# Kernel optimization log

Hardware: AMD Instinct MI355X
Metric: run time of the kernel (lower is better)

## Reference

```python
import jax, jax.numpy as jnp
import numpy as np

B, H, W, C, FD, HID = 64, 128, 128, 10, 32, 64
OFFSETS = [(-1,-1),(-1,0),(-1,1),(0,-1),(0,1),(1,-1),(1,0),(1,1)]

def setup_inputs() -> dict:
    key = jax.random.key(0)
    ks = jax.random.split(key, 13)
    s = lambda n: 1.0 / np.sqrt(n)
    return {
        "beliefs": jax.random.normal(ks[0], (B, H, W, C), jnp.float32),
        "constraints": jax.random.uniform(ks[1], (B, H, W, 8, 3), jnp.float32),
        "filename_embed": jax.random.normal(ks[2], (B, FD), jnp.float32),
        # message_net: Linear(2C+3+FD -> HID), ReLU, Linear(HID -> C)
        "mw1": jax.random.uniform(ks[3], (2*C+3+FD, HID), jnp.float32, -s(2*C+3+FD), s(2*C+3+FD)),
        "mb1": jax.random.uniform(ks[4], (HID,), jnp.float32, -s(2*C+3+FD), s(2*C+3+FD)),
        "mw2": jax.random.uniform(ks[5], (HID, C), jnp.float32, -s(HID), s(HID)),
        "mb2": jax.random.uniform(ks[6], (C,), jnp.float32, -s(HID), s(HID)),
        # update_net: Linear(2C -> HID), ReLU, Linear(HID -> C)
        "uw1": jax.random.uniform(ks[7], (2*C, HID), jnp.float32, -s(2*C), s(2*C)),
        "ub1": jax.random.uniform(ks[8], (HID,), jnp.float32, -s(2*C), s(2*C)),
        "uw2": jax.random.uniform(ks[9], (HID, C), jnp.float32, -s(HID), s(HID)),
        "ub2": jax.random.uniform(ks[10], (C,), jnp.float32, -s(HID), s(HID)),
        "gamma": jnp.ones((C,), jnp.float32),
        "beta": jnp.zeros((C,), jnp.float32),
    }

def reference(beliefs, constraints, filename_embed, mw1, mb1, mw2, mb2, uw1, ub1, uw2, ub2, gamma, beta):
    b, h, w, c = beliefs.shape
    # replicate-pad spatial dims (matches F.pad mode='replicate')
    bp = jnp.pad(beliefs, ((0,0),(1,1),(1,1),(0,0)), mode='edge')
    # gather 8 neighbors -> [B,H,W,8,C]
    neigh = jnp.stack([bp[:, 1+dy:1+dy+h, 1+dx:1+dx+w, :] for dy, dx in OFFSETS], axis=3)
    self_b = jnp.broadcast_to(beliefs[:, :, :, None, :], (b, h, w, 8, c))
    fn = jnp.broadcast_to(filename_embed[:, None, None, None, :], (b, h, w, 8, filename_embed.shape[-1]))
    msg_in = jnp.concatenate([self_b, neigh, constraints, fn], axis=-1)  # [B,H,W,8,2C+3+FD]
    msgs = jax.nn.relu(msg_in @ mw1 + mb1) @ mw2 + mb2                   # [B,H,W,8,C]
    agg = msgs.mean(axis=3)                                              # [B,H,W,C]
    upd_in = jnp.concatenate([beliefs, agg], axis=-1)
    upd = jax.nn.relu(upd_in @ uw1 + ub1) @ uw2 + ub2
    x = beliefs + 0.5 * upd
    mu = x.mean(-1, keepdims=True)
    var = ((x - mu) ** 2).mean(-1, keepdims=True)
    return (x - mu) * jax.lax.rsqrt(var + 1e-5) * gamma + beta
```

## Files before the change

### kernel.cpp

```cpp
#include <hip/hip_runtime.h>
#include <hip/hip_bf16.h>

typedef unsigned int u32;
typedef _Float16 h2 __attribute__((ext_vector_type(2)));

#define TILE 16
#define HALO 18
#define NPIX (HALO*HALO)
#define NBSTRIDE 36

#define W_SELF   0
#define W_NBW    320
#define W_WC     640
#define W_MW2    736
#define W_UB1    1056
#define W_UW1    1088
#define W_UW2    1728
#define WS_W     2048
#define WS_SCAL  4096
#define WS_DWORDS 4136

__device__ __forceinline__ h2 pkrtz(float a, float b) {
    return __builtin_bit_cast(h2, __builtin_amdgcn_cvt_pkrtz(a, b));
}
#if __has_builtin(__builtin_elementwise_fma)
__device__ __forceinline__ h2 pkfma(h2 a, h2 b, h2 c) { return __builtin_elementwise_fma(a, b, c); }
#else
extern "C" __device__ h2 __ocml_fma_2f16(h2, h2, h2);
__device__ __forceinline__ h2 pkfma(h2 a, h2 b, h2 c) { return __ocml_fma_2f16(a, b, c); }
#endif
__device__ __forceinline__ float dot2f(h2 a, h2 b, float c) {
#if __has_builtin(__builtin_amdgcn_fdot2)
    return __builtin_amdgcn_fdot2(__builtin_bit_cast(__attribute__((ext_vector_type(2))) __fp16, a),
                                  __builtin_bit_cast(__attribute__((ext_vector_type(2))) __fp16, b),
                                  c, false);
#else
    return fmaf((float)a.x, (float)b.x, fmaf((float)a.y, (float)b.y, c));
#endif
}
__device__ __forceinline__ h2 relu2(h2 v) {
    h2 z = (h2)(_Float16)0;
#if __has_builtin(__builtin_elementwise_max)
    return __builtin_elementwise_max(v, z);
#else
    h2 r;
    r.x = v.x > (_Float16)0 ? v.x : (_Float16)0;
    r.y = v.y > (_Float16)0 ? v.y : (_Float16)0;
    return r;
#endif
}
__device__ __forceinline__ h2 h2cast(u32 v) { return __builtin_bit_cast(h2, v); }

__global__ __launch_bounds__(64) void prep_kernel(
    const float* __restrict__ fn,  const float* __restrict__ mw1, const float* __restrict__ mb1,
    const float* __restrict__ mw2, const float* __restrict__ mb2, const float* __restrict__ uw1,
    const float* __restrict__ ub1, const float* __restrict__ uw2, const float* __restrict__ ub2,
    const float* __restrict__ gam, const float* __restrict__ bet, u32* __restrict__ ws)
{
    const int b = blockIdx.x, t = threadIdx.x;
    h2* wh = (h2*)ws;
    if (t < 32) {
        float a0 = mb1[2*t], a1 = mb1[2*t+1];
        for (int f = 0; f < 32; f++) {
            float fv = fn[b*32 + f];
            a0 += fv * mw1[(23+f)*64 + 2*t];
            a1 += fv * mw1[(23+f)*64 + 2*t+1];
        }
        wh[b*32 + t] = pkrtz(a0, a1);
    }
    if (b == 0) {
        for (int i = t; i < 2048; i += 64) {
            float a, c; int j;
            if      (i < 320)  { int cc = i>>5,  hp = i&31;  a = mw1[cc*64 + 2*hp];       c = mw1[cc*64 + 2*hp+1]; }
            else if (i < 640)  { j = i-320;  int q = j>>6, hh = j&63; a = mw1[(10+2*q)*64 + hh]; c = mw1[(11+2*q)*64 + hh]; }
            else if (i < 736)  { j = i-640;  int r = j>>5, hp = j&31; a = mw1[(20+r)*64 + 2*hp]; c = mw1[(20+r)*64 + 2*hp+1]; }
            else if (i < 1056) { j = i-736;  int cc = j>>5, hp = j&31; a = mw2[(2*hp)*10 + cc];  c = mw2[(2*hp+1)*10 + cc]; }
            else if (i < 1088) { j = i-1056; a = ub1[2*j]; c = ub1[2*j+1]; }
            else if (i < 1728) { j = i-1088; int cc = j>>5, hp = j&31; a = uw1[cc*64 + 2*hp];    c = uw1[cc*64 + 2*hp+1]; }
            else               { j = i-1728; int cc = j>>5, hp = j&31; a = uw2[(2*hp)*10 + cc];  c = uw2[(2*hp+1)*10 + cc]; }
            wh[WS_W + i] = pkrtz(a, c);
        }
        if (t < 40) {
            float v;
            if      (t < 10) v = mb2[t];
            else if (t < 20) v = ub2[t-10];
            else if (t < 30) v = gam[t-20];
            else             v = bet[t-30];
            ((float*)ws)[WS_SCAL + t] = v;
        }
    }
}

__global__ __launch_bounds__(256, 3) void mp_kernel(
    const float* __restrict__ beliefs, const float* __restrict__ cons,
    const u32* __restrict__ ws, float* __restrict__ out)
{
    __shared__ h2 bel_s[NPIX*5];
    __shared__ __align__(16) u32 nbp_u[NPIX*NBSTRIDE];

    const int tid = threadIdx.x;
    const int b = blockIdx.z, y0 = blockIdx.y*TILE, x0 = blockIdx.x*TILE;

    const h2* Wfnb = (const h2*)ws;
    const h2* W    = ((const h2*)ws) + WS_W;
    const float* SC = ((const float*)ws) + WS_SCAL;

    for (int i = tid; i < NPIX*5; i += 256) {
        int p = i/5, q = i - p*5;
        int py = p/HALO, px = p - py*HALO;
        int gy = y0-1+py; gy = gy<0?0:(gy>127?127:gy);
        int gx = x0-1+px; gx = gx<0?0:(gx>127?127:gx);
        const float2 v = *(const float2*)(beliefs + (size_t)((b*128+gy)*128+gx)*10 + 2*q);
        bel_s[i] = pkrtz(v.x, v.y);
    }
    __syncthreads();

    for (int p = tid; p < NPIX; p += 256) {
        h2 bc[5];
        #pragma unroll
        for (int q = 0; q < 5; q++) bc[q] = bel_s[p*5 + q];
        #pragma unroll 4
        for (int hp = 0; hp < 32; hp++) {
            float a0 = 0.f, a1 = 0.f;
            #pragma unroll
            for (int q = 0; q < 5; q++) {
                a0 = dot2f(bc[q], W[W_NBW + q*64 + 2*hp],     a0);
                a1 = dot2f(bc[q], W[W_NBW + q*64 + 2*hp + 1], a1);
            }
            nbp_u[p*NBSTRIDE + hp] = __builtin_bit_cast(u32, pkrtz(a0, a1));
        }
    }
    __syncthreads();

    const int tx = tid & 15, ty = tid >> 4;
    const int pc = (ty+1)*HALO + (tx+1);
    const size_t gpix = (size_t)((b*128 + (y0+ty))*128 + (x0+tx));

    int p36[8];
    {
        const int doff[8] = {-19,-18,-17,-1,1,17,18,19};
        #pragma unroll
        for (int k = 0; k < 8; k++) p36[k] = (pc + doff[k]) * NBSTRIDE;
    }

    float bel[10]; h2 beld[10];
    {
        const float2* bp = (const float2*)(beliefs + gpix*10);
        #pragma unroll
        for (int q = 0; q < 5; q++) {
            float2 v = bp[q];
            bel[2*q] = v.x; bel[2*q+1] = v.y;
            beld[2*q]   = pkrtz(v.x, v.x);
            beld[2*q+1] = pkrtz(v.y, v.y);
        }
    }
    h2 cond[24];
    {
        const float4* cp = (const float4*)(cons + gpix*24);
        #pragma unroll
        for (int r = 0; r < 6; r++) {
            float4 v = cp[r];
            cond[4*r+0] = pkrtz(v.x, v.x);
            cond[4*r+1] = pkrtz(v.y, v.y);
            cond[4*r+2] = pkrtz(v.z, v.z);
            cond[4*r+3] = pkrtz(v.w, v.w);
        }
    }

    float acc2[10];
    #pragma unroll
    for (int c = 0; c < 10; c++) acc2[c] = 0.f;

    #pragma unroll 2
    for (int ch = 0; ch < 8; ch++) {
        const int hb = 4*ch;
        h2 t01[4], s01[4];
        #pragma unroll
        for (int j = 0; j < 4; j++) { t01[j] = Wfnb[b*32 + hb + j]; s01[j] = (h2)(_Float16)0; }
        #pragma unroll
        for (int c = 0; c < 10; c++) {
            #pragma unroll
            for (int j = 0; j < 4; j++)
                t01[j] = pkfma(beld[c], W[W_SELF + c*32 + hb + j], t01[j]);
        }
        h2 wc0[4], wc1[4], wc2[4];
        #pragma unroll
        for (int j = 0; j < 4; j++) {
            wc0[j] = W[W_WC      + hb + j];
            wc1[j] = W[W_WC + 32 + hb + j];
            wc2[j] = W[W_WC + 64 + hb + j];
        }
        #pragma unroll
        for (int k = 0; k < 8; k++) {
            const uint4 nv = *(const uint4*)(nbp_u + p36[k] + hb);
            const h2 nb[4] = { h2cast(nv.x), h2cast(nv.y), h2cast(nv.z), h2cast(nv.w) };
            const h2 c0 = cond[k*3+0], c1 = cond[k*3+1], c2 = cond[k*3+2];
            #pragma unroll
            for (int j = 0; j < 4; j++) {
                h2 v = t01[j] + nb[j];
                v = pkfma(c0, wc0[j], v);
                v = pkfma(c1, wc1[j], v);
                v = pkfma(c2, wc2[j], v);
                s01[j] += relu2(v);
            }
        }
        #pragma unroll
        for (int c = 0; c < 10; c++) {
            #pragma unroll
            for (int j = 0; j < 4; j++)
                acc2[c] = dot2f(s01[j], W[W_MW2 + c*32 + hb + j], acc2[c]);
        }
    }

    h2 aggd[10];
    #pragma unroll
    for (int c = 0; c < 10; c++) {
        float a = acc2[c]*0.125f + SC[c];
        aggd[c] = pkrtz(a, a);
    }

    float od[10];
    #pragma unroll
    for (int c = 0; c < 10; c++) od[c] = 0.f;

    #pragma unroll 4
    for (int hp = 0; hp < 32; hp++) {
        h2 u01 = W[W_UB1 + hp];
        #pragma unroll
        for (int c = 0; c < 10; c++) u01 = pkfma(beld[c], W[W_UW1 + c*32 + hp], u01);
        #pragma unroll
        for (int c = 0; c < 10; c++) u01 = pkfma(aggd[c], W[W_UW1 + (10+c)*32 + hp], u01);
        u01 = relu2(u01);
        #pragma unroll
        for (int c = 0; c < 10; c++) od[c] = dot2f(u01, W[W_UW2 + c*32 + hp], od[c]);
    }

    float x[10], mu = 0.f;
    #pragma unroll
    for (int c = 0; c < 10; c++) { x[c] = bel[c] + 0.5f*(od[c] + SC[10+c]); mu += x[c]; }
    mu *= 0.1f;
    float var = 0.f;
    #pragma unroll
    for (int c = 0; c < 10; c++) { float d = x[c] - mu; var += d*d; }
    var *= 0.1f;
    const float rs = rsqrtf(var + 1e-5f);

    float2* op = (float2*)(out + gpix*10);
    #pragma unroll
    for (int q = 0; q < 5; q++) {
        float2 r;
        r.x = (x[2*q]   - mu)*rs*SC[20+2*q]   + SC[30+2*q];
        r.y = (x[2*q+1] - mu)*rs*SC[20+2*q+1] + SC[30+2*q+1];
        op[q] = r;
    }
}

__device__ __forceinline__ float bf_lo(u32 v) { return __uint_as_float(v << 16); }
__device__ __forceinline__ float bf_hi(u32 v) { return __uint_as_float(v & 0xffff0000u); }
__device__ __forceinline__ u32 f2bf(float f) {
    u32 u = __float_as_uint(f);
    return (u + 0x7fffu + ((u >> 16) & 1u)) >> 16;
}
__device__ __forceinline__ u32 pack2(float a, float b) { return f2bf(a) | (f2bf(b) << 16); }
__device__ __forceinline__ u32 fpair(const float* a, int pi) { return pack2(a[2*pi], a[2*pi+1]); }

#define FW_MW2 736
#define FW_MB2 1056
#define FW_UW1 1061
#define FW_UB1 1701
#define FW_UW2 1733
#define FW_UB2 2053
#define FW_GAM 2058
#define FW_BET 2063
#define FW_TOT 2068

__global__ __launch_bounds__(256) void fallback_kernel(
    const float* __restrict__ beliefs, const float* __restrict__ cons, const float* __restrict__ fn,
    const float* __restrict__ mw1, const float* __restrict__ mb1, const float* __restrict__ mw2,
    const float* __restrict__ mb2, const float* __restrict__ uw1, const float* __restrict__ ub1,
    const float* __restrict__ uw2, const float* __restrict__ ub2, const float* __restrict__ gam,
    const float* __restrict__ bet, float* __restrict__ out)
{
    __shared__ float bel_s[NPIX*10];
    __shared__ u32   nbp_s[32*NPIX];
    __shared__ u32   w_s[FW_TOT];
    __shared__ float fnb_s[64];

    const int tid = threadIdx.x;
    const int b  = blockIdx.z;
    const int y0 = blockIdx.y * TILE;
    const int x0 = blockIdx.x * TILE;

    for (int i = tid; i < FW_TOT; i += 256) {
        u32 v;
        if      (i < 736)  v = fpair(mw1, i);
        else if (i < 1056) v = fpair(mw2, i - 736);
        else if (i < 1061) v = fpair(mb2, i - 1056);
        else if (i < 1701) v = fpair(uw1, i - 1061);
        else if (i < 1733) v = fpair(ub1, i - 1701);
        else if (i < 2053) v = fpair(uw2, i - 1733);
        else if (i < 2058) v = fpair(ub2, i - 2053);
        else if (i < 2063) v = fpair(gam, i - 2058);
        else               v = fpair(bet, i - 2063);
        w_s[i] = v;
    }
    if (tid < 64) {
        float acc = mb1[tid];
        #pragma unroll 8
        for (int f = 0; f < 32; f++)
            acc += fn[b*32 + f] * mw1[(23 + f)*64 + tid];
        fnb_s[tid] = acc;
    }
    for (int idx = tid; idx < NPIX*10; idx += 256) {
        int p = idx/10, c = idx - p*10;
        int py = p/HALO, px = p - py*HALO;
        int gy = y0-1+py; gy = gy<0?0:(gy>127?127:gy);
        int gx = x0-1+px; gx = gx<0?0:(gx>127?127:gx);
        bel_s[idx] = beliefs[((size_t)(b*128+gy)*128+gx)*10 + c];
    }
    __syncthreads();

    for (int p = tid; p < NPIX; p += 256) {
        float bl[10];
        #pragma unroll
        for (int c = 0; c < 10; c++) bl[c] = bel_s[p*10 + c];
        #pragma unroll 4
        for (int hp = 0; hp < 32; hp++) {
            float t0 = 0.f, t1 = 0.f;
            #pragma unroll
            for (int c = 0; c < 10; c++) {
                u32 wv = w_s[(10 + c)*32 + hp];
                t0 += bl[c] * bf_lo(wv);
                t1 += bl[c] * bf_hi(wv);
            }
            nbp_s[hp*NPIX + p] = pack2(t0, t1);
        }
    }
    __syncthreads();

    const int tx = tid & 15, ty = tid >> 4;
    const int pc = (ty + 1)*HALO + (tx + 1);
    float bel[10];
    #pragma unroll
    for (int c = 0; c < 10; c++) bel[c] = bel_s[pc*10 + c];
    const size_t gpix = (size_t)(b*128 + (y0 + ty))*128 + (x0 + tx);
    float con[24];
    #pragma unroll
    for (int j = 0; j < 24; j++) con[j] = cons[gpix*24 + j];

    float acc2[10];
    #pragma unroll
    for (int c = 0; c < 10; c++) acc2[c] = 0.f;

    #pragma unroll 2
    for (int hp = 0; hp < 32; hp++) {
        const int h0 = 2*hp, h1 = h0 + 1;
        float t0 = fnb_s[h0], t1 = fnb_s[h1];
        #pragma unroll
        for (int c = 0; c < 10; c++) {
            u32 wv = w_s[c*32 + hp];
            t0 += bel[c] * bf_lo(wv);
            t1 += bel[c] * bf_hi(wv);
        }
        const u32 wc0 = w_s[20*32 + hp], wc1 = w_s[21*32 + hp], wc2 = w_s[22*32 + hp];
        const u32* nbb = nbp_s + hp*NPIX + pc - 19;
        float s0 = 0.f, s1 = 0.f;
        #pragma unroll
        for (int k = 0; k < 8; k++) {
            const int doff[8] = { 0, 1, 2, 18, 20, 36, 37, 38 };
            u32 nv = nbb[doff[k]];
            float c0 = con[k*3], c1 = con[k*3+1], c2 = con[k*3+2];
            float v0 = t0 + bf_lo(nv) + c0*bf_lo(wc0) + c1*bf_lo(wc1) + c2*bf_lo(wc2);
            float v1 = t1 + bf_hi(nv) + c0*bf_hi(wc0) + c1*bf_hi(wc1) + c2*bf_hi(wc2);
            s0 += fmaxf(v0, 0.f);
            s1 += fmaxf(v1, 0.f);
        }
        #pragma unroll
        for (int cq = 0; cq < 5; cq++) {
            u32 a0 = w_s[FW_MW2 + h0*5 + cq];
            u32 a1 = w_s[FW_MW2 + h1*5 + cq];
            acc2[2*cq]   += s0*bf_lo(a0) + s1*bf_lo(a1);
            acc2[2*cq+1] += s0*bf_hi(a0) + s1*bf_hi(a1);
        }
    }

    float agg[10];
    #pragma unroll
    for (int cq = 0; cq < 5; cq++) {
        u32 bp = w_s[FW_MB2 + cq];
        agg[2*cq]   = acc2[2*cq]  *0.125f + bf_lo(bp);
        agg[2*cq+1] = acc2[2*cq+1]*0.125f + bf_hi(bp);
    }

    float od[10];
    #pragma unroll
    for (int c = 0; c < 10; c++) od[c] = 0.f;
    #pragma unroll 2
    for (int hp = 0; hp < 32; hp++) {
        u32 ubp = w_s[FW_UB1 + hp];
        float u0 = bf_lo(ubp), u1 = bf_hi(ubp);
        #pragma unroll
        for (int c = 0; c < 10; c++) {
            u32 wv = w_s[FW_UW1 + c*32 + hp];
            u0 += bel[c] * bf_lo(wv);
            u1 += bel[c] * bf_hi(wv);
        }
        #pragma unroll
        for (int c = 0; c < 10; c++) {
            u32 wv = w_s[FW_UW1 + (10 + c)*32 + hp];
            u0 += agg[c] * bf_lo(wv);
            u1 += agg[c] * bf_hi(wv);
        }
        u0 = fmaxf(u0, 0.f); u1 = fmaxf(u1, 0.f);
        const int h0 = 2*hp, h1 = h0 + 1;
        #pragma unroll
        for (int cq = 0; cq < 5; cq++) {
            u32 a0 = w_s[FW_UW2 + h0*5 + cq];
            u32 a1 = w_s[FW_UW2 + h1*5 + cq];
            od[2*cq]   += u0*bf_lo(a0) + u1*bf_lo(a1);
            od[2*cq+1] += u0*bf_hi(a0) + u1*bf_hi(a1);
        }
    }

    float x[10], mu = 0.f;
    #pragma unroll
    for (int cq = 0; cq < 5; cq++) {
        u32 bp = w_s[FW_UB2 + cq];
        x[2*cq]   = bel[2*cq]   + 0.5f*(od[2*cq]   + bf_lo(bp));
        x[2*cq+1] = bel[2*cq+1] + 0.5f*(od[2*cq+1] + bf_hi(bp));
        mu += x[2*cq] + x[2*cq+1];
    }
    mu *= 0.1f;
    float var = 0.f;
    #pragma unroll
    for (int c = 0; c < 10; c++) { float d = x[c] - mu; var += d*d; }
    var *= 0.1f;
    const float rs = rsqrtf(var + 1e-5f);

    float2* op = reinterpret_cast<float2*>(out + gpix*10);
    #pragma unroll
    for (int q = 0; q < 5; q++) {
        u32 gp = w_s[FW_GAM + q], bq = w_s[FW_BET + q];
        float2 r;
        r.x = (x[2*q]   - mu)*rs*bf_lo(gp) + bf_lo(bq);
        r.y = (x[2*q+1] - mu)*rs*bf_hi(gp) + bf_hi(bq);
        op[q] = r;
    }
}

extern "C" void kernel_launch(void* const* d_in, const int* in_sizes, int n_in,
                              void* d_out, int out_size, void* d_ws, size_t ws_size,
                              hipStream_t stream) {
    (void)in_sizes; (void)n_in; (void)out_size;
    const float* beliefs = (const float*)d_in[0];
    const float* cons    = (const float*)d_in[1];
    const float* fn      = (const float*)d_in[2];
    const float* mw1     = (const float*)d_in[3];
    const float* mb1     = (const float*)d_in[4];
    const float* mw2     = (const float*)d_in[5];
    const float* mb2     = (const float*)d_in[6];
    const float* uw1     = (const float*)d_in[7];
    const float* ub1     = (const float*)d_in[8];
    const float* uw2     = (const float*)d_in[9];
    const float* ub2     = (const float*)d_in[10];
    const float* gam     = (const float*)d_in[11];
    const float* bet     = (const float*)d_in[12];
    float* outp = (float*)d_out;

    if (ws_size >= (size_t)WS_DWORDS*4) {
        prep_kernel<<<dim3(64), dim3(64), 0, stream>>>(
            fn, mw1, mb1, mw2, mb2, uw1, ub1, uw2, ub2, gam, bet, (u32*)d_ws);
        mp_kernel<<<dim3(8, 8, 64), dim3(256), 0, stream>>>(
            beliefs, cons, (const u32*)d_ws, outp);
    } else {
        fallback_kernel<<<dim3(8, 8, 64), dim3(256), 0, stream>>>(
            beliefs, cons, fn, mw1, mb1, mw2, mb2, uw1, ub1, uw2, ub2, gam, bet, outp);
    }
}
```

Baseline: 321.1 us.

## Split neighbor projection into two hidden halves to cut LDS and raise occupancy

The shared neighbor-projection buffer is restructured into a chunk-major layout holding only half of the hidden units at a time. It is computed and consumed in two passes with a barrier between them, and the bel_s staging buffer is dropped by reading halo beliefs straight from global memory. The smaller LDS footprint lets launch bounds target 6 blocks per CU instead of 3. The prep kernel also spreads weight packing across all blocks instead of block 0. The cost is halo beliefs being loaded twice, extra barriers, and more register pressure under the tighter occupancy bound.

```diff
diff --git a/kernel.cpp b/kernel.cpp
--- a/kernel.cpp
+++ b/kernel.cpp
@@ -7,7 +7,6 @@
 #define TILE 16
 #define HALO 18
 #define NPIX (HALO*HALO)
-#define NBSTRIDE 36
 
 #define W_SELF   0
 #define W_NBW    320
@@ -61,42 +60,40 @@
     h2* wh = (h2*)ws;
     if (t < 32) {
         float a0 = mb1[2*t], a1 = mb1[2*t+1];
+        #pragma unroll 8
         for (int f = 0; f < 32; f++) {
             float fv = fn[b*32 + f];
             a0 += fv * mw1[(23+f)*64 + 2*t];
             a1 += fv * mw1[(23+f)*64 + 2*t+1];
         }
         wh[b*32 + t] = pkrtz(a0, a1);
-    }
-    if (b == 0) {
-        for (int i = t; i < 2048; i += 64) {
-            float a, c; int j;
-            if      (i < 320)  { int cc = i>>5,  hp = i&31;  a = mw1[cc*64 + 2*hp];       c = mw1[cc*64 + 2*hp+1]; }
-            else if (i < 640)  { j = i-320;  int q = j>>6, hh = j&63; a = mw1[(10+2*q)*64 + hh]; c = mw1[(11+2*q)*64 + hh]; }
-            else if (i < 736)  { j = i-640;  int r = j>>5, hp = j&31; a = mw1[(20+r)*64 + 2*hp]; c = mw1[(20+r)*64 + 2*hp+1]; }
-            else if (i < 1056) { j = i-736;  int cc = j>>5, hp = j&31; a = mw2[(2*hp)*10 + cc];  c = mw2[(2*hp+1)*10 + cc]; }
-            else if (i < 1088) { j = i-1056; a = ub1[2*j]; c = ub1[2*j+1]; }
-            else if (i < 1728) { j = i-1088; int cc = j>>5, hp = j&31; a = uw1[cc*64 + 2*hp];    c = uw1[cc*64 + 2*hp+1]; }
-            else               { j = i-1728; int cc = j>>5, hp = j&31; a = uw2[(2*hp)*10 + cc];  c = uw2[(2*hp+1)*10 + cc]; }
-            wh[WS_W + i] = pkrtz(a, c);
-        }
-        if (t < 40) {
-            float v;
-            if      (t < 10) v = mb2[t];
-            else if (t < 20) v = ub2[t-10];
-            else if (t < 30) v = gam[t-20];
-            else             v = bet[t-30];
-            ((float*)ws)[WS_SCAL + t] = v;
-        }
-    }
-}
-
-__global__ __launch_bounds__(256, 3) void mp_kernel(
+    } else {
+        const int i = b*32 + (t - 32);
+        float a, c; int j;
+        if      (i < 320)  { int cc = i>>5,  hp = i&31;  a = mw1[cc*64 + 2*hp];       c = mw1[cc*64 + 2*hp+1]; }
+        else if (i < 640)  { j = i-320;  int q = j>>6, hh = j&63; a = mw1[(10+2*q)*64 + hh]; c = mw1[(11+2*q)*64 + hh]; }
+        else if (i < 736)  { j = i-640;  int r = j>>5, hp = j&31; a = mw1[(20+r)*64 + 2*hp]; c = mw1[(20+r)*64 + 2*hp+1]; }
+        else if (i < 1056) { j = i-736;  int cc = j>>5, hp = j&31; a = mw2[(2*hp)*10 + cc];  c = mw2[(2*hp+1)*10 + cc]; }
+        else if (i < 1088) { j = i-1056; a = ub1[2*j]; c = ub1[2*j+1]; }
+        else if (i < 1728) { j = i-1088; int cc = j>>5, hp = j&31; a = uw1[cc*64 + 2*hp];    c = uw1[cc*64 + 2*hp+1]; }
+        else               { j = i-1728; int cc = j>>5, hp = j&31; a = uw2[(2*hp)*10 + cc];  c = uw2[(2*hp+1)*10 + cc]; }
+        wh[WS_W + i] = pkrtz(a, c);
+    }
+    if (b == 0 && t < 40) {
+        float v;
+        if      (t < 10) v = mb2[t];
+        else if (t < 20) v = ub2[t-10];
+        else if (t < 30) v = gam[t-20];
+        else             v = bet[t-30];
+        ((float*)ws)[WS_SCAL + t] = v;
+    }
+}
+
+__global__ __launch_bounds__(256, 6) void mp_kernel(
     const float* __restrict__ beliefs, const float* __restrict__ cons,
     const u32* __restrict__ ws, float* __restrict__ out)
 {
-    __shared__ h2 bel_s[NPIX*5];
-    __shared__ __align__(16) u32 nbp_u[NPIX*NBSTRIDE];
+    __shared__ __align__(16) u32 nbp_u[4*NPIX*4];
 
     const int tid = threadIdx.x;
     const int b = blockIdx.z, y0 = blockIdx.y*TILE, x0 = blockIdx.x*TILE;
@@ -105,42 +102,15 @@
     const h2* W    = ((const h2*)ws) + WS_W;
     const float* SC = ((const float*)ws) + WS_SCAL;
 
-    for (int i = tid; i < NPIX*5; i += 256) {
-        int p = i/5, q = i - p*5;
-        int py = p/HALO, px = p - py*HALO;
-        int gy = y0-1+py; gy = gy<0?0:(gy>127?127:gy);
-        int gx = x0-1+px; gx = gx<0?0:(gx>127?127:gx);
-        const float2 v = *(const float2*)(beliefs + (size_t)((b*128+gy)*128+gx)*10 + 2*q);
-        bel_s[i] = pkrtz(v.x, v.y);
-    }
-    __syncthreads();
-
-    for (int p = tid; p < NPIX; p += 256) {
-        h2 bc[5];
-        #pragma unroll
-        for (int q = 0; q < 5; q++) bc[q] = bel_s[p*5 + q];
-        #pragma unroll 4
-        for (int hp = 0; hp < 32; hp++) {
-            float a0 = 0.f, a1 = 0.f;
-            #pragma unroll
-            for (int q = 0; q < 5; q++) {
-                a0 = dot2f(bc[q], W[W_NBW + q*64 + 2*hp],     a0);
-                a1 = dot2f(bc[q], W[W_NBW + q*64 + 2*hp + 1], a1);
-            }
-            nbp_u[p*NBSTRIDE + hp] = __builtin_bit_cast(u32, pkrtz(a0, a1));
-        }
-    }
-    __syncthreads();
-
     const int tx = tid & 15, ty = tid >> 4;
     const int pc = (ty+1)*HALO + (tx+1);
     const size_t gpix = (size_t)((b*128 + (y0+ty))*128 + (x0+tx));
 
-    int p36[8];
+    int pnb[8];
     {
         const int doff[8] = {-19,-18,-17,-1,1,17,18,19};
         #pragma unroll
-        for (int k = 0; k < 8; k++) p36[k] = (pc + doff[k]) * NBSTRIDE;
+        for (int k = 0; k < 8; k++) pnb[k] = pc + doff[k];
     }
 
     float bel[10]; h2 beld[10];
@@ -171,44 +141,75 @@
     #pragma unroll
     for (int c = 0; c < 10; c++) acc2[c] = 0.f;
 
-    #pragma unroll 2
-    for (int ch = 0; ch < 8; ch++) {
-        const int hb = 4*ch;
-        h2 t01[4], s01[4];
-        #pragma unroll
-        for (int j = 0; j < 4; j++) { t01[j] = Wfnb[b*32 + hb + j]; s01[j] = (h2)(_Float16)0; }
-        #pragma unroll
-        for (int c = 0; c < 10; c++) {
-            #pragma unroll
-            for (int j = 0; j < 4; j++)
-                t01[j] = pkfma(beld[c], W[W_SELF + c*32 + hb + j], t01[j]);
-        }
-        h2 wc0[4], wc1[4], wc2[4];
-        #pragma unroll
-        for (int j = 0; j < 4; j++) {
-            wc0[j] = W[W_WC      + hb + j];
-            wc1[j] = W[W_WC + 32 + hb + j];
-            wc2[j] = W[W_WC + 64 + hb + j];
-        }
-        #pragma unroll
-        for (int k = 0; k < 8; k++) {
-            const uint4 nv = *(const uint4*)(nbp_u + p36[k] + hb);
-            const h2 nb[4] = { h2cast(nv.x), h2cast(nv.y), h2cast(nv.z), h2cast(nv.w) };
-            const h2 c0 = cond[k*3+0], c1 = cond[k*3+1], c2 = cond[k*3+2];
+    for (int half = 0; half < 2; half++) {
+        if (half) __syncthreads();
+
+        for (int p = tid; p < NPIX; p += 256) {
+            int py = p/HALO, px = p - py*HALO;
+            int gy = y0-1+py; gy = gy<0?0:(gy>127?127:gy);
+            int gx = x0-1+px; gx = gx<0?0:(gx>127?127:gx);
+            const float2* bp = (const float2*)(beliefs + (size_t)((b*128+gy)*128+gx)*10);
+            h2 bc[5];
+            #pragma unroll
+            for (int q = 0; q < 5; q++) { float2 v = bp[q]; bc[q] = pkrtz(v.x, v.y); }
+            #pragma unroll
+            for (int cl = 0; cl < 4; cl++) {
+                u32 ov[4];
+                #pragma unroll
+                for (int j = 0; j < 4; j++) {
+                    const int hp = half*16 + cl*4 + j;
+                    float a0 = 0.f, a1 = 0.f;
+                    #pragma unroll
+                    for (int q = 0; q < 5; q++) {
+                        a0 = dot2f(bc[q], W[W_NBW + q*64 + 2*hp],     a0);
+                        a1 = dot2f(bc[q], W[W_NBW + q*64 + 2*hp + 1], a1);
+                    }
+                    ov[j] = __builtin_bit_cast(u32, pkrtz(a0, a1));
+                }
+                *(uint4*)(nbp_u + ((cl*NPIX + p) << 2)) = make_uint4(ov[0], ov[1], ov[2], ov[3]);
+            }
+        }
+        __syncthreads();
+
+        #pragma unroll 2
+        for (int cl = 0; cl < 4; cl++) {
+            const int hb = half*16 + cl*4;
+            h2 t01[4], s01[4];
+            #pragma unroll
+            for (int j = 0; j < 4; j++) { t01[j] = Wfnb[b*32 + hb + j]; s01[j] = (h2)(_Float16)0; }
+            #pragma unroll
+            for (int c = 0; c < 10; c++) {
+                #pragma unroll
+                for (int j = 0; j < 4; j++)
+                    t01[j] = pkfma(beld[c], W[W_SELF + c*32 + hb + j], t01[j]);
+            }
+            h2 wc0[4], wc1[4], wc2[4];
             #pragma unroll
             for (int j = 0; j < 4; j++) {
-                h2 v = t01[j] + nb[j];
-                v = pkfma(c0, wc0[j], v);
-                v = pkfma(c1, wc1[j], v);
-                v = pkfma(c2, wc2[j], v);
-                s01[j] += relu2(v);
-            }
-        }
-        #pragma unroll
-        for (int c = 0; c < 10; c++) {
-            #pragma unroll
-            for (int j = 0; j < 4; j++)
-                acc2[c] = dot2f(s01[j], W[W_MW2 + c*32 + hb + j], acc2[c]);
+                wc0[j] = W[W_WC      + hb + j];
+                wc1[j] = W[W_WC + 32 + hb + j];
+                wc2[j] = W[W_WC + 64 + hb + j];
+            }
+            #pragma unroll
+            for (int k = 0; k < 8; k++) {
+                const uint4 nv = *(const uint4*)(nbp_u + ((cl*NPIX + pnb[k]) << 2));
+                const h2 nb[4] = { h2cast(nv.x), h2cast(nv.y), h2cast(nv.z), h2cast(nv.w) };
+                const h2 c0 = cond[k*3+0], c1 = cond[k*3+1], c2 = cond[k*3+2];
+                #pragma unroll
+                for (int j = 0; j < 4; j++) {
+                    h2 v = t01[j] + nb[j];
+                    v = pkfma(c0, wc0[j], v);
+                    v = pkfma(c1, wc1[j], v);
+                    v = pkfma(c2, wc2[j], v);
+                    s01[j] += relu2(v);
+                }
+            }
+            #pragma unroll
+            for (int c = 0; c < 10; c++) {
+                #pragma unroll
+                for (int j = 0; j < 4; j++)
+                    acc2[c] = dot2f(s01[j], W[W_MW2 + c*32 + hb + j], acc2[c]);
+            }
         }
     }
 
```

New measurement: 310.6 us. 3.3% less time.
